# Optimization experiments

Measured on AMD Instinct MI355X. Metric: run time of the kernel, lower is better.

The kernel has to match this reference:

```python
import jax, jax.numpy as jnp
import numpy as np

BN_EPS = 1e-5
SMOOTH = 10.0


def l2norm(x, eps=1e-8):
    return x / (jnp.linalg.norm(x, axis=-1, keepdims=True) + eps)


def bn_tanh(z, gamma, beta):
    # BatchNorm1d in training mode (batch statistics, biased variance) + tanh
    mu = z.mean(axis=0)
    var = ((z - mu) ** 2).mean(axis=0)
    return jnp.tanh(gamma * (z - mu) / jnp.sqrt(var + BN_EPS) + beta)


def setup_inputs() -> dict:
    key = jax.random.key(0)
    ks = jax.random.split(key, 6)
    B, S, E, D = 1024, 512, 1024, 2048  # batch, att_num, embed_dim, image_dim
    return {
        "emb_instance": jax.random.normal(ks[0], (B, E), jnp.float32),
        "concept_feature": jax.random.normal(ks[1], (S, D), jnp.float32),
        "GT_label": jax.random.normal(ks[2], (B, S), jnp.float32),
        "fc1_w": jax.random.normal(ks[3], (D, E), jnp.float32) * 0.02,
        "fc1_b": jnp.zeros((E,), jnp.float32),
        "bn1_g": jnp.ones((E,), jnp.float32),
        "bn1_b": jnp.zeros((E,), jnp.float32),
        "fc2_w": jax.random.normal(ks[4], (E, E), jnp.float32) * 0.02,
        "fc2_b": jnp.zeros((E,), jnp.float32),
        "bn2_g": jnp.ones((E,), jnp.float32),
        "bn2_b": jnp.zeros((E,), jnp.float32),
        "fc3_w": jax.random.normal(ks[5], (E,), jnp.float32) * 0.02,
        "fc3_b": jnp.zeros((1,), jnp.float32),
        "GT_label_ratio": 0,
    }


def reference(emb_instance, concept_feature, GT_label, fc1_w, fc1_b, bn1_g, bn1_b,
              fc2_w, fc2_b, bn2_g, bn2_b, fc3_w, fc3_b, GT_label_ratio):
    # input_modal == 'visual' path
    W_s = bn_tanh(concept_feature @ fc1_w + fc1_b, bn1_g, bn1_b)   # (S, E)
    W_v = bn_tanh(emb_instance @ fc2_w + fc2_b, bn2_g, bn2_b)      # (B, E)
    # Fused bilinear score: fc3(W_s * W_v) == (W_v * fc3_w) @ W_s^T + fc3_b
    # avoids materializing the (B, S, E) broadcast intermediate.
    a_s = jnp.einsum('be,se->bs', W_v * fc3_w, W_s) + fc3_b        # (B, S)
    weights_v = jax.nn.softmax(a_s * SMOOTH, axis=1)
    cf = l2norm(concept_feature)                                    # (S, D)
    emb_concept = l2norm(weights_v @ cf)                            # (B, D)
    return (emb_concept, weights_v)
```

## Files before the change

kernel.cpp:

```cpp
#include <hip/hip_runtime.h>
#include <hip/hip_bf16.h>
#include <math.h>

#define B_ 1024
#define S_ 512
#define E_ 1024
#define D_ 2048
#define SMOOTH 10.0f

typedef __attribute__((ext_vector_type(8))) short bf16x8;
typedef __attribute__((ext_vector_type(4))) float f32x4;

__device__ __forceinline__ short f2bf(float f) {
    __hip_bfloat16 h = __float2bfloat16(f);
    short s; __builtin_memcpy(&s, &h, 2); return s;
}

__device__ __forceinline__ void gload16(const short* g, short* l) {
    __builtin_amdgcn_global_load_lds(
        (const __attribute__((address_space(1))) void*)(g),
        (__attribute__((address_space(3))) void*)(l), 16, 0, 0);
}

__inline__ __device__ float waveReduceMax(float v) {
#pragma unroll
    for (int o = 32; o; o >>= 1) v = fmaxf(v, __shfl_xor(v, o));
    return v;
}
__inline__ __device__ float waveReduceSum(float v) {
#pragma unroll
    for (int o = 32; o; o >>= 1) v += __shfl_xor(v, o);
    return v;
}

struct KArgs {
    const float *cf, *emb, *fc1w, *fc2w, *bn1g, *bn1b, *bn2g, *bn2b, *fc3w;
    short *A1, *A2, *Bt1, *Bt2, *cfT, *Ws, *Wv3, *A4;
    float *invn, *Z1, *Z2, *part1, *part2, *P1, *P2, *P3, *emb_pre;
    float *weights_v, *emb_concept;
};

__device__ __forceinline__ void transpose_bf(const float* __restrict__ in,
                                             short* __restrict__ out,
                                             int C, int r0, int c0, int ldo,
                                             int tid, float (*t)[33]) {
    int cx = tid & 31, ry0 = tid >> 5;
#pragma unroll
    for (int i = 0; i < 4; i++) {
        int ry = ry0 + i * 8;
        t[ry][cx] = in[(size_t)(r0 + ry) * C + c0 + cx];
    }
    __syncthreads();
    int rx = tid & 31, cy0 = tid >> 5;
#pragma unroll
    for (int i = 0; i < 4; i++) {
        int cy = cy0 + i * 8;
        out[(size_t)(c0 + cy) * ldo + r0 + rx] = f2bf(t[rx][cy]);
    }
}

__global__ __launch_bounds__(256) void prep_k(KArgs a) {
    __shared__ float t[32][33];
    __shared__ float red[4];
    const int task = blockIdx.x;
    const int tid = threadIdx.x;
    if (task < 512) {
        int row = task;
        const float* x = a.cf + (size_t)row * D_;
        short* aa = a.A1 + (size_t)row * D_;
        float ss = 0.f;
#pragma unroll
        for (int j = 0; j < 8; j++) {
            int i = j * 256 + tid;
            float v = x[i];
            aa[i] = f2bf(v);
            ss += v * v;
        }
        ss = waveReduceSum(ss);
        if ((tid & 63) == 0) red[tid >> 6] = ss;
        __syncthreads();
        if (tid == 0) {
            float s = red[0] + red[1] + red[2] + red[3];
            a.invn[row] = 1.0f / (sqrtf(s) + 1e-8f);
        }
    } else if (task < 1024) {
        int r0 = (task - 512) * 2;
#pragma unroll
        for (int rr = 0; rr < 2; rr++) {
            int row = r0 + rr;
            const float* x = a.emb + (size_t)row * E_;
            short* aa = a.A2 + (size_t)row * E_;
#pragma unroll
            for (int j = 0; j < 4; j++) {
                int i = j * 256 + tid;
                aa[i] = f2bf(x[i]);
            }
        }
    } else if (task < 3072) {
        int b2 = task - 1024;
        int c0 = (b2 & 31) * 32;
        int r0 = (b2 >> 5) * 32;
        transpose_bf(a.fc1w, a.Bt1, E_, r0, c0, D_, tid, t);
    } else if (task < 4096) {
        int b2 = task - 3072;
        int c0 = (b2 & 31) * 32;
        int r0 = (b2 >> 5) * 32;
        transpose_bf(a.fc2w, a.Bt2, E_, r0, c0, E_, tid, t);
    } else {
        int b2 = task - 4096;
        int c0 = (b2 & 63) * 32;
        int r0 = (b2 >> 6) * 32;
        transpose_bf(a.cf, a.cfT, D_, r0, c0, S_, tid, t);
    }
}

struct GP {
    const short* A;
    const short* Bm;
    float* P;
    int M, N, K, Kc, nx, ny;
};

__device__ __forceinline__ void gemm128_core(const GP g, int bid, short* lds) {
    const int tid = threadIdx.x;
    const int per = g.nx * g.ny;
    const int z = bid / per, rem = bid % per;
    const int by = rem / g.nx, bx = rem % g.nx;
    const int bm = by * 128, bn = bx * 128;
    const int kz = z * g.Kc;
    float* C = g.P + (size_t)z * g.M * g.N;
    const short* gA = g.A + (size_t)bm * g.K + kz;
    const short* gB = g.Bm + (size_t)bn * g.K + kz;

    size_t soff[4];
#pragma unroll
    for (int i = 0; i < 4; i++) {
        int ci = tid + i * 256;
        int row = ci >> 3, c = ci & 7;
        soff[i] = (size_t)row * g.K + ((c ^ (row & 7)) << 3);
    }

    auto stage = [&](int buf, int kt) {
        short* base = lds + buf * 16384;
#pragma unroll
        for (int i = 0; i < 4; i++) {
            gload16(gA + soff[i] + kt, base + tid * 8 + i * 2048);
            gload16(gB + soff[i] + kt, base + 8192 + tid * 8 + i * 2048);
        }
    };

    const int lane = tid & 63, wid = tid >> 6;
    const int wr = wid >> 1, wc = wid & 1;
    const int r16 = lane & 15, kg = lane >> 4;
    const int rs7 = (r16 & 7);

    f32x4 acc[4][4] = {};
    const int nt = g.Kc >> 6;

    stage(0, 0);
    for (int t = 0; t < nt; ++t) {
        __syncthreads();
        if (t + 1 < nt) stage((t + 1) & 1, (t + 1) << 6);
        const short* LA = lds + (t & 1) * 16384;
        const short* LB = LA + 8192;
#pragma unroll
        for (int ks = 0; ks < 2; ++ks) {
            const int sw = ((ks * 4 + kg) ^ rs7) << 3;
            bf16x8 a[4], b[4];
#pragma unroll
            for (int m = 0; m < 4; m++)
                a[m] = *(const bf16x8*)(LA + (wr * 64 + m * 16 + r16) * 64 + sw);
#pragma unroll
            for (int n = 0; n < 4; n++)
                b[n] = *(const bf16x8*)(LB + (wc * 64 + n * 16 + r16) * 64 + sw);
#pragma unroll
            for (int m = 0; m < 4; m++)
#pragma unroll
                for (int n = 0; n < 4; n++)
                    acc[m][n] = __builtin_amdgcn_mfma_f32_16x16x32_bf16(a[m], b[n], acc[m][n], 0, 0, 0);
        }
    }

#pragma unroll
    for (int m = 0; m < 4; m++)
#pragma unroll
        for (int n = 0; n < 4; n++) {
            int col = bn + wc * 64 + n * 16 + r16;
#pragma unroll
            for (int r = 0; r < 4; r++) {
                int row = bm + wr * 64 + m * 16 + kg * 4 + r;
                C[(size_t)row * g.N + col] = acc[m][n][r];
            }
        }
}

__global__ __launch_bounds__(256) void gemm_dual(GP g0, GP g1, int n0) {
    __shared__ short lds[32768];
    int bid = blockIdx.x;
    if (bid < n0) gemm128_core(g0, bid, lds);
    else gemm128_core(g1, bid - n0, lds);
}

__global__ __launch_bounds__(256) void gemm_one(GP g) {
    __shared__ short lds[32768];
    gemm128_core(g, blockIdx.x, lds);
}

__global__ __launch_bounds__(256) void bn_stats12(KArgs a) {
    int c = blockIdx.x * 256 + threadIdx.x;
    if (blockIdx.y < 32) {
        int r0 = blockIdx.y * 16;
        float s = 0.f, ss = 0.f;
        for (int r = r0; r < r0 + 16; r++) {
            float z = 0.f;
#pragma unroll
            for (int k = 0; k < 4; k++) z += a.P1[(size_t)k * S_ * E_ + (size_t)r * E_ + c];
            a.Z1[(size_t)r * E_ + c] = z;
            s += z; ss += z * z;
        }
        a.part1[(size_t)blockIdx.y * 2 * E_ + c] = s;
        a.part1[(size_t)blockIdx.y * 2 * E_ + E_ + c] = ss;
    } else {
        int y2 = blockIdx.y - 32;
        int r0 = y2 * 32;
        float s = 0.f, ss = 0.f;
        for (int r = r0; r < r0 + 32; r++) {
            float z = 0.f;
#pragma unroll
            for (int k = 0; k < 2; k++) z += a.P2[(size_t)k * B_ * E_ + (size_t)r * E_ + c];
            a.Z2[(size_t)r * E_ + c] = z;
            s += z; ss += z * z;
        }
        a.part2[(size_t)y2 * 2 * E_ + c] = s;
        a.part2[(size_t)y2 * 2 * E_ + E_ + c] = ss;
    }
}

__global__ __launch_bounds__(256) void bn_apply12(KArgs a) {
    int c = blockIdx.x * 256 + threadIdx.x;
    bool br1 = blockIdx.y < 32;
    const float* part = br1 ? a.part1 : a.part2;
    float s = 0.f, ss = 0.f;
#pragma unroll
    for (int k = 0; k < 32; k++) {
        s += part[(size_t)k * 2 * E_ + c];
        ss += part[(size_t)k * 2 * E_ + E_ + c];
    }
    float invR = br1 ? (1.0f / 512.0f) : (1.0f / 1024.0f);
    float mu = s * invR;
    float var = ss * invR - mu * mu;
    float rstd = rsqrtf(var + 1e-5f);
    float Aa = (br1 ? a.bn1g[c] : a.bn2g[c]) * rstd;
    float Bb = (br1 ? a.bn1b[c] : a.bn2b[c]) - Aa * mu;
    float sc = br1 ? 1.0f : a.fc3w[c];
    const float* Z = br1 ? a.Z1 : a.Z2;
    short* W = br1 ? a.Ws : a.Wv3;
    int nr = br1 ? 16 : 32;
    int r0 = (br1 ? blockIdx.y : (blockIdx.y - 32)) * nr;
    for (int r = r0; r < r0 + nr; r++) {
        float w = tanhf(fmaf(Z[(size_t)r * E_ + c], Aa, Bb)) * sc;
        W[(size_t)r * E_ + c] = f2bf(w);
    }
}

__global__ __launch_bounds__(256) void softmax_k(KArgs a) {
    __shared__ float red[4];
    int row = blockIdx.x;
    int tid = threadIdx.x;
    float v0 = 0.f, v1 = 0.f;
#pragma unroll
    for (int k = 0; k < 4; k++) {
        v0 += a.P3[(size_t)k * B_ * S_ + (size_t)row * S_ + tid];
        v1 += a.P3[(size_t)k * B_ * S_ + (size_t)row * S_ + tid + 256];
    }
    v0 *= SMOOTH;
    v1 *= SMOOTH;
    float m = waveReduceMax(fmaxf(v0, v1));
    if ((tid & 63) == 0) red[tid >> 6] = m;
    __syncthreads();
    m = fmaxf(fmaxf(red[0], red[1]), fmaxf(red[2], red[3]));
    float e0 = __expf(v0 - m), e1 = __expf(v1 - m);
    float s = waveReduceSum(e0 + e1);
    __syncthreads();
    if ((tid & 63) == 0) red[tid >> 6] = s;
    __syncthreads();
    s = red[0] + red[1] + red[2] + red[3];
    float inv = 1.0f / s;
    float w0 = e0 * inv, w1 = e1 * inv;
    a.weights_v[(size_t)row * S_ + tid] = w0;
    a.weights_v[(size_t)row * S_ + tid + 256] = w1;
    a.A4[(size_t)row * S_ + tid] = f2bf(w0 * a.invn[tid]);
    a.A4[(size_t)row * S_ + tid + 256] = f2bf(w1 * a.invn[tid + 256]);
}

__global__ __launch_bounds__(256) void rownorm_k(KArgs a) {
    __shared__ float red[4];
    int row = blockIdx.x;
    int tid = threadIdx.x;
    float v[8];
    float ss = 0.f;
#pragma unroll
    for (int j = 0; j < 8; j++) {
        v[j] = a.emb_pre[(size_t)row * D_ + j * 256 + tid];
        ss += v[j] * v[j];
    }
    ss = waveReduceSum(ss);
    if ((tid & 63) == 0) red[tid >> 6] = ss;
    __syncthreads();
    ss = red[0] + red[1] + red[2] + red[3];
    float sc = 1.0f / (sqrtf(ss) + 1e-8f);
#pragma unroll
    for (int j = 0; j < 8; j++)
        a.emb_concept[(size_t)row * D_ + j * 256 + tid] = v[j] * sc;
}

extern "C" void kernel_launch(void* const* d_in, const int* in_sizes, int n_in,
                              void* d_out, int out_size, void* d_ws, size_t ws_size,
                              hipStream_t stream) {
    float* out = (float*)d_out;
    const size_t MB = 1024 * 1024;
    char* w = (char*)d_ws;

    KArgs a;
    a.cf   = (const float*)d_in[1];
    a.emb  = (const float*)d_in[0];
    a.fc1w = (const float*)d_in[3];
    a.fc2w = (const float*)d_in[7];
    a.bn1g = (const float*)d_in[5];
    a.bn1b = (const float*)d_in[6];
    a.bn2g = (const float*)d_in[9];
    a.bn2b = (const float*)d_in[10];
    a.fc3w = (const float*)d_in[11];
    a.Bt1  = (short*)(w + 0 * MB);
    a.Bt2  = (short*)(w + 4 * MB);
    a.A1   = (short*)(w + 6 * MB);
    a.A2   = (short*)(w + 8 * MB);
    a.cfT  = (short*)(w + 10 * MB);
    a.Z1   = (float*)(w + 12 * MB);
    a.Z2   = (float*)(w + 14 * MB);
    a.Ws   = (short*)(w + 18 * MB);
    a.Wv3  = (short*)(w + 19 * MB);
    a.A4   = (short*)(w + 21 * MB);
    a.part1 = (float*)(w + 22 * MB);
    a.part2 = (float*)(w + 22 * MB + 512 * 1024);
    a.invn  = (float*)(w + 23 * MB);
    a.P1   = (float*)(w + 24 * MB);
    a.P2   = (float*)(w + 32 * MB);
    a.P3   = (float*)(w + 24 * MB);
    a.emb_pre = (float*)(w + 32 * MB);
    a.emb_concept = out;
    a.weights_v   = out + (size_t)B_ * D_;

    prep_k<<<5120, 256, 0, stream>>>(a);

    GP g1 = {a.A1, a.Bt1, a.P1, S_, E_, D_, 512, 8, 4};
    GP g2 = {a.A2, a.Bt2, a.P2, B_, E_, E_, 512, 8, 8};
    gemm_dual<<<256, 256, 0, stream>>>(g1, g2, 128);

    bn_stats12<<<dim3(4, 64), 256, 0, stream>>>(a);
    bn_apply12<<<dim3(4, 64), 256, 0, stream>>>(a);

    GP g3 = {a.Wv3, a.Ws, a.P3, B_, S_, E_, 256, 4, 8};
    gemm_one<<<128, 256, 0, stream>>>(g3);

    softmax_k<<<B_, 256, 0, stream>>>(a);

    GP g4 = {a.A4, a.cfT, a.emb_pre, B_, D_, S_, 512, 16, 8};
    gemm_one<<<128, 256, 0, stream>>>(g4);

    rownorm_k<<<B_, 256, 0, stream>>>(a);
}
```

Measured before the change: 74.80 us.

## Drop split-K in GEMMs, fuse BN stats/apply, halve prep grid

Removes the split-K partitioning from the fc1, fc2 and score GEMMs, so each block writes final outputs directly. This eliminates the partial-sum buffers and the reduction passes in BN stats and softmax. The two BN kernels are merged into one kernel that reduces column statistics in shared memory and then applies tanh. The prep kernel now runs each block over two tasks. The trade-off is far fewer GEMM blocks (96 and 32 on a GPU with many CUs), each with a longer K loop, which risks underutilising the device.

Result: slower. 103.9 us (+38.9%).

```diff
diff --git a/kernel.cpp b/kernel.cpp
--- a/kernel.cpp
+++ b/kernel.cpp
@@ -36,7 +36,7 @@
 struct KArgs {
     const float *cf, *emb, *fc1w, *fc2w, *bn1g, *bn1b, *bn2g, *bn2b, *fc3w;
     short *A1, *A2, *Bt1, *Bt2, *cfT, *Ws, *Wv3, *A4;
-    float *invn, *Z1, *Z2, *part1, *part2, *P1, *P2, *P3, *emb_pre;
+    float *invn, *Z1, *Z2, *a_s, *emb_pre;
     float *weights_v, *emb_concept;
 };
 
@@ -59,11 +59,8 @@
     }
 }
 
-__global__ __launch_bounds__(256) void prep_k(KArgs a) {
-    __shared__ float t[32][33];
-    __shared__ float red[4];
-    const int task = blockIdx.x;
-    const int tid = threadIdx.x;
+__device__ __forceinline__ void prep_task(const KArgs& a, int task, int tid,
+                                          float (*t)[33], float* red) {
     if (task < 512) {
         int row = task;
         const float* x = a.cf + (size_t)row * D_;
@@ -114,6 +111,15 @@
     }
 }
 
+__global__ __launch_bounds__(256) void prep_k(KArgs a) {
+    __shared__ float t[32][33];
+    __shared__ float red[4];
+    for (int it = 0; it < 2; ++it) {
+        prep_task(a, blockIdx.x + it * 2560, threadIdx.x, t, red);
+        __syncthreads();
+    }
+}
+
 struct GP {
     const short* A;
     const short* Bm;
@@ -206,58 +212,41 @@
     gemm128_core(g, blockIdx.x, lds);
 }
 
-__global__ __launch_bounds__(256) void bn_stats12(KArgs a) {
-    int c = blockIdx.x * 256 + threadIdx.x;
-    if (blockIdx.y < 32) {
-        int r0 = blockIdx.y * 16;
-        float s = 0.f, ss = 0.f;
-        for (int r = r0; r < r0 + 16; r++) {
-            float z = 0.f;
-#pragma unroll
-            for (int k = 0; k < 4; k++) z += a.P1[(size_t)k * S_ * E_ + (size_t)r * E_ + c];
-            a.Z1[(size_t)r * E_ + c] = z;
-            s += z; ss += z * z;
-        }
-        a.part1[(size_t)blockIdx.y * 2 * E_ + c] = s;
-        a.part1[(size_t)blockIdx.y * 2 * E_ + E_ + c] = ss;
-    } else {
-        int y2 = blockIdx.y - 32;
-        int r0 = y2 * 32;
-        float s = 0.f, ss = 0.f;
-        for (int r = r0; r < r0 + 32; r++) {
-            float z = 0.f;
-#pragma unroll
-            for (int k = 0; k < 2; k++) z += a.P2[(size_t)k * B_ * E_ + (size_t)r * E_ + c];
-            a.Z2[(size_t)r * E_ + c] = z;
-            s += z; ss += z * z;
-        }
-        a.part2[(size_t)y2 * 2 * E_ + c] = s;
-        a.part2[(size_t)y2 * 2 * E_ + E_ + c] = ss;
-    }
-}
-
-__global__ __launch_bounds__(256) void bn_apply12(KArgs a) {
-    int c = blockIdx.x * 256 + threadIdx.x;
-    bool br1 = blockIdx.y < 32;
-    const float* part = br1 ? a.part1 : a.part2;
+__global__ __launch_bounds__(256) void bn_fused(KArgs a) {
+    __shared__ float rs[16][16], rss[16][16];
+    __shared__ float sAa[16], sBb[16], sSc[16];
+    const int tid = threadIdx.x;
+    const int col = tid & 15, rg = tid >> 4;
+    const int c = blockIdx.x * 16 + col;
+    const bool br1 = (blockIdx.y == 0);
+    const float* Z = br1 ? a.Z1 : a.Z2;
+    const int R = br1 ? S_ : B_;
+
     float s = 0.f, ss = 0.f;
-#pragma unroll
-    for (int k = 0; k < 32; k++) {
-        s += part[(size_t)k * 2 * E_ + c];
-        ss += part[(size_t)k * 2 * E_ + E_ + c];
-    }
-    float invR = br1 ? (1.0f / 512.0f) : (1.0f / 1024.0f);
-    float mu = s * invR;
-    float var = ss * invR - mu * mu;
-    float rstd = rsqrtf(var + 1e-5f);
-    float Aa = (br1 ? a.bn1g[c] : a.bn2g[c]) * rstd;
-    float Bb = (br1 ? a.bn1b[c] : a.bn2b[c]) - Aa * mu;
-    float sc = br1 ? 1.0f : a.fc3w[c];
-    const float* Z = br1 ? a.Z1 : a.Z2;
+    for (int r = rg; r < R; r += 16) {
+        float z = Z[(size_t)r * E_ + c];
+        s += z; ss += z * z;
+    }
+    rs[rg][col] = s;
+    rss[rg][col] = ss;
+    __syncthreads();
+    if (rg == 0) {
+        float S = 0.f, SS = 0.f;
+#pragma unroll
+        for (int k = 0; k < 16; k++) { S += rs[k][col]; SS += rss[k][col]; }
+        float invR = 1.0f / (float)R;
+        float mu = S * invR;
+        float var = SS * invR - mu * mu;
+        float rstd = rsqrtf(var + 1e-5f);
+        float Aa = (br1 ? a.bn1g[c] : a.bn2g[c]) * rstd;
+        sAa[col] = Aa;
+        sBb[col] = (br1 ? a.bn1b[c] : a.bn2b[c]) - Aa * mu;
+        sSc[col] = br1 ? 1.0f : a.fc3w[c];
+    }
+    __syncthreads();
+    float Aa = sAa[col], Bb = sBb[col], sc = sSc[col];
     short* W = br1 ? a.Ws : a.Wv3;
-    int nr = br1 ? 16 : 32;
-    int r0 = (br1 ? blockIdx.y : (blockIdx.y - 32)) * nr;
-    for (int r = r0; r < r0 + nr; r++) {
+    for (int r = rg; r < R; r += 16) {
         float w = tanhf(fmaf(Z[(size_t)r * E_ + c], Aa, Bb)) * sc;
         W[(size_t)r * E_ + c] = f2bf(w);
     }
@@ -267,14 +256,8 @@
     __shared__ float red[4];
     int row = blockIdx.x;
     int tid = threadIdx.x;
-    float v0 = 0.f, v1 = 0.f;
-#pragma unroll
-    for (int k = 0; k < 4; k++) {
-        v0 += a.P3[(size_t)k * B_ * S_ + (size_t)row * S_ + tid];
-        v1 += a.P3[(size_t)k * B_ * S_ + (size_t)row * S_ + tid + 256];
-    }
-    v0 *= SMOOTH;
-    v1 *= SMOOTH;
+    float v0 = a.a_s[(size_t)row * S_ + tid] * SMOOTH;
+    float v1 = a.a_s[(size_t)row * S_ + tid + 256] * SMOOTH;
     float m = waveReduceMax(fmaxf(v0, v1));
     if ((tid & 63) == 0) red[tid >> 6] = m;
     __syncthreads();
@@ -341,31 +324,26 @@
     a.Ws   = (short*)(w + 18 * MB);
     a.Wv3  = (short*)(w + 19 * MB);
     a.A4   = (short*)(w + 21 * MB);
-    a.part1 = (float*)(w + 22 * MB);
-    a.part2 = (float*)(w + 22 * MB + 512 * 1024);
-    a.invn  = (float*)(w + 23 * MB);
-    a.P1   = (float*)(w + 24 * MB);
-    a.P2   = (float*)(w + 32 * MB);
-    a.P3   = (float*)(w + 24 * MB);
-    a.emb_pre = (float*)(w + 32 * MB);
+    a.invn = (float*)(w + 22 * MB);
+    a.a_s  = (float*)(w + 23 * MB);
+    a.emb_pre = (float*)(w + 25 * MB);
     a.emb_concept = out;
     a.weights_v   = out + (size_t)B_ * D_;
 
-    prep_k<<<5120, 256, 0, stream>>>(a);
-
-    GP g1 = {a.A1, a.Bt1, a.P1, S_, E_, D_, 512, 8, 4};
-    GP g2 = {a.A2, a.Bt2, a.P2, B_, E_, E_, 512, 8, 8};
-    gemm_dual<<<256, 256, 0, stream>>>(g1, g2, 128);
-
-    bn_stats12<<<dim3(4, 64), 256, 0, stream>>>(a);
-    bn_apply12<<<dim3(4, 64), 256, 0, stream>>>(a);
-
-    GP g3 = {a.Wv3, a.Ws, a.P3, B_, S_, E_, 256, 4, 8};
-    gemm_one<<<128, 256, 0, stream>>>(g3);
+    prep_k<<<2560, 256, 0, stream>>>(a);
+
+    GP g1 = {a.A1, a.Bt1, a.Z1, S_, E_, D_, D_, 8, 4};
+    GP g2 = {a.A2, a.Bt2, a.Z2, B_, E_, E_, E_, 8, 8};
+    gemm_dual<<<96, 256, 0, stream>>>(g1, g2, 32);
+
+    bn_fused<<<dim3(64, 2), 256, 0, stream>>>(a);
+
+    GP g3 = {a.Wv3, a.Ws, a.a_s, B_, S_, E_, E_, 4, 8};
+    gemm_one<<<32, 256, 0, stream>>>(g3);
 
     softmax_k<<<B_, 256, 0, stream>>>(a);
 
-    GP g4 = {a.A4, a.cfT, a.emb_pre, B_, D_, S_, 512, 16, 8};
+    GP g4 = {a.A4, a.cfT, a.emb_pre, B_, D_, S_, S_, 16, 8};
     gemm_one<<<128, 256, 0, stream>>>(g4);
 
     rownorm_k<<<B_, 256, 0, stream>>>(a);
```

## Replace split-K fc GEMMs with 64x128 tiles and fuse BN stats into epilogue

Applied to the files above, without the earlier changes.

The fc1/fc2 GEMMs switch from split-K 128x128 tiles to full-K 64x128 tiles. The epilogue writes Z directly and computes per-column partial sums and sums of squares through shuffles and LDS. This removes the split-K partial buffers and the separate bn_stats kernel that reduced them, saving a launch and a large amount of global traffic. The prep kernel and the transposes also move to vectorized 16-byte loads and 8-byte stores. In exchange, fc1 blocks now loop over the full K=2048 with only 192 blocks launched, which lowers parallelism and leaves fc1 and fc2 blocks with uneven amounts of work.

After: 73.77 us. Within noise of the previous version (-1.4%).

```diff
diff --git a/kernel.cpp b/kernel.cpp
--- a/kernel.cpp
+++ b/kernel.cpp
@@ -9,6 +9,7 @@
 #define SMOOTH 10.0f
 
 typedef __attribute__((ext_vector_type(8))) short bf16x8;
+typedef __attribute__((ext_vector_type(4))) short s16x4;
 typedef __attribute__((ext_vector_type(4))) float f32x4;
 
 __device__ __forceinline__ short f2bf(float f) {
@@ -36,7 +37,7 @@
 struct KArgs {
     const float *cf, *emb, *fc1w, *fc2w, *bn1g, *bn1b, *bn2g, *bn2b, *fc3w;
     short *A1, *A2, *Bt1, *Bt2, *cfT, *Ws, *Wv3, *A4;
-    float *invn, *Z1, *Z2, *part1, *part2, *P1, *P2, *P3, *emb_pre;
+    float *invn, *Z1, *Z2, *part1, *part2, *P3, *emb_pre;
     float *weights_v, *emb_concept;
 };
 
@@ -44,18 +45,19 @@
                                              short* __restrict__ out,
                                              int C, int r0, int c0, int ldo,
                                              int tid, float (*t)[33]) {
-    int cx = tid & 31, ry0 = tid >> 5;
-#pragma unroll
-    for (int i = 0; i < 4; i++) {
-        int ry = ry0 + i * 8;
-        t[ry][cx] = in[(size_t)(r0 + ry) * C + c0 + cx];
-    }
-    __syncthreads();
-    int rx = tid & 31, cy0 = tid >> 5;
-#pragma unroll
-    for (int i = 0; i < 4; i++) {
-        int cy = cy0 + i * 8;
-        out[(size_t)(c0 + cy) * ldo + r0 + rx] = f2bf(t[rx][cy]);
+    {
+        int r = tid >> 3, cq = tid & 7;
+        f32x4 v = *(const f32x4*)(in + (size_t)(r0 + r) * C + c0 + cq * 4);
+#pragma unroll
+        for (int i = 0; i < 4; i++) t[r][cq * 4 + i] = v[i];
+    }
+    __syncthreads();
+    {
+        int rq = tid & 7, cy = tid >> 3;
+        s16x4 o;
+#pragma unroll
+        for (int i = 0; i < 4; i++) o[i] = f2bf(t[rq * 4 + i][cy]);
+        *(s16x4*)(out + (size_t)(c0 + cy) * ldo + r0 + rq * 4) = o;
     }
 }
 
@@ -70,11 +72,13 @@
         short* aa = a.A1 + (size_t)row * D_;
         float ss = 0.f;
 #pragma unroll
-        for (int j = 0; j < 8; j++) {
-            int i = j * 256 + tid;
-            float v = x[i];
-            aa[i] = f2bf(v);
-            ss += v * v;
+        for (int j = 0; j < 2; j++) {
+            int i = (j * 256 + tid) * 4;
+            f32x4 v = *(const f32x4*)(x + i);
+            s16x4 o;
+#pragma unroll
+            for (int q = 0; q < 4; q++) { o[q] = f2bf(v[q]); ss += v[q] * v[q]; }
+            *(s16x4*)(aa + i) = o;
         }
         ss = waveReduceSum(ss);
         if ((tid & 63) == 0) red[tid >> 6] = ss;
@@ -88,13 +92,12 @@
 #pragma unroll
         for (int rr = 0; rr < 2; rr++) {
             int row = r0 + rr;
-            const float* x = a.emb + (size_t)row * E_;
-            short* aa = a.A2 + (size_t)row * E_;
-#pragma unroll
-            for (int j = 0; j < 4; j++) {
-                int i = j * 256 + tid;
-                aa[i] = f2bf(x[i]);
-            }
+            int i = tid * 4;
+            f32x4 v = *(const f32x4*)(a.emb + (size_t)row * E_ + i);
+            s16x4 o;
+#pragma unroll
+            for (int q = 0; q < 4; q++) o[q] = f2bf(v[q]);
+            *(s16x4*)(a.A2 + (size_t)row * E_ + i) = o;
         }
     } else if (task < 3072) {
         int b2 = task - 1024;
@@ -114,6 +117,135 @@
     }
 }
 
+struct GP64 {
+    const short* A;
+    const short* Bm;
+    float* Z;
+    float* part;
+    int M, N, K, nx;
+};
+
+__device__ __forceinline__ void gemm64_core(const GP64 g, int bid, short* lds) {
+    const int tid = threadIdx.x;
+    const int by = bid / g.nx, bx = bid % g.nx;
+    const int bm = by * 64, bn = bx * 128;
+    const short* gA = g.A + (size_t)bm * g.K;
+    const short* gB = g.Bm + (size_t)bn * g.K;
+
+    size_t aoff[2], boff[4];
+#pragma unroll
+    for (int i = 0; i < 2; i++) {
+        int ci = tid + i * 256;
+        int row = ci >> 3, c = ci & 7;
+        aoff[i] = (size_t)row * g.K + ((c ^ (row & 7)) << 3);
+    }
+#pragma unroll
+    for (int i = 0; i < 4; i++) {
+        int ci = tid + i * 256;
+        int row = ci >> 3, c = ci & 7;
+        boff[i] = (size_t)row * g.K + ((c ^ (row & 7)) << 3);
+    }
+
+    auto stage = [&](int buf, int kt) {
+        short* base = lds + buf * 12288;
+#pragma unroll
+        for (int i = 0; i < 2; i++)
+            gload16(gA + aoff[i] + kt, base + tid * 8 + i * 2048);
+#pragma unroll
+        for (int i = 0; i < 4; i++)
+            gload16(gB + boff[i] + kt, base + 4096 + tid * 8 + i * 2048);
+    };
+
+    const int lane = tid & 63, wid = tid >> 6;
+    const int wr = wid >> 1, wc = wid & 1;
+    const int r16 = lane & 15, kg = lane >> 4;
+    const int rs7 = r16 & 7;
+
+    f32x4 acc[2][4] = {};
+    const int nt = g.K >> 6;
+
+    stage(0, 0);
+    for (int t = 0; t < nt; ++t) {
+        __syncthreads();
+        if (t + 1 < nt) stage((t + 1) & 1, (t + 1) << 6);
+        const short* LA = lds + (t & 1) * 12288;
+        const short* LB = LA + 4096;
+#pragma unroll
+        for (int ks = 0; ks < 2; ++ks) {
+            const int sw = ((ks * 4 + kg) ^ rs7) << 3;
+            bf16x8 av[2], bv[4];
+#pragma unroll
+            for (int m = 0; m < 2; m++)
+                av[m] = *(const bf16x8*)(LA + (wr * 32 + m * 16 + r16) * 64 + sw);
+#pragma unroll
+            for (int n = 0; n < 4; n++)
+                bv[n] = *(const bf16x8*)(LB + (wc * 64 + n * 16 + r16) * 64 + sw);
+#pragma unroll
+            for (int m = 0; m < 2; m++)
+#pragma unroll
+                for (int n = 0; n < 4; n++)
+                    acc[m][n] = __builtin_amdgcn_mfma_f32_16x16x32_bf16(av[m], bv[n], acc[m][n], 0, 0, 0);
+        }
+    }
+
+#pragma unroll
+    for (int m = 0; m < 2; m++)
+#pragma unroll
+        for (int n = 0; n < 4; n++) {
+            int col = bn + wc * 64 + n * 16 + r16;
+#pragma unroll
+            for (int r = 0; r < 4; r++) {
+                int row = bm + wr * 32 + m * 16 + kg * 4 + r;
+                g.Z[(size_t)row * g.N + col] = acc[m][n][r];
+            }
+        }
+
+    float cs[4], cq[4];
+#pragma unroll
+    for (int n = 0; n < 4; n++) {
+        float s = 0.f, q = 0.f;
+#pragma unroll
+        for (int m = 0; m < 2; m++)
+#pragma unroll
+            for (int r = 0; r < 4; r++) {
+                float v = acc[m][n][r];
+                s += v; q += v * v;
+            }
+        cs[n] = s; cq[n] = q;
+    }
+#pragma unroll
+    for (int n = 0; n < 4; n++) {
+        cs[n] += __shfl_xor(cs[n], 16); cq[n] += __shfl_xor(cq[n], 16);
+        cs[n] += __shfl_xor(cs[n], 32); cq[n] += __shfl_xor(cq[n], 32);
+    }
+    __syncthreads();
+    float* sred = (float*)lds;
+    if (kg == 0) {
+#pragma unroll
+        for (int n = 0; n < 4; n++) {
+            int idx = (((wr * 2 + wc) * 4 + n) * 16 + r16) * 2;
+            sred[idx] = cs[n];
+            sred[idx + 1] = cq[n];
+        }
+    }
+    __syncthreads();
+    if (tid < 128) {
+        int wcc = tid >> 6, n = (tid >> 4) & 3, r = tid & 15;
+        int i0 = (((0 * 2 + wcc) * 4 + n) * 16 + r) * 2;
+        int i1 = (((1 * 2 + wcc) * 4 + n) * 16 + r) * 2;
+        int col = bn + wcc * 64 + n * 16 + r;
+        g.part[(size_t)by * 2 * g.N + col] = sred[i0] + sred[i1];
+        g.part[(size_t)by * 2 * g.N + g.N + col] = sred[i0 + 1] + sred[i1 + 1];
+    }
+}
+
+__global__ __launch_bounds__(256) void gemm_dual64(GP64 g0, GP64 g1, int n0) {
+    __shared__ short lds[24576];
+    int bid = blockIdx.x;
+    if (bid < n0) gemm64_core(g0, bid, lds);
+    else gemm64_core(g1, bid - n0, lds);
+}
+
 struct GP {
     const short* A;
     const short* Bm;
@@ -194,55 +326,18 @@
         }
 }
 
-__global__ __launch_bounds__(256) void gemm_dual(GP g0, GP g1, int n0) {
-    __shared__ short lds[32768];
-    int bid = blockIdx.x;
-    if (bid < n0) gemm128_core(g0, bid, lds);
-    else gemm128_core(g1, bid - n0, lds);
-}
-
 __global__ __launch_bounds__(256) void gemm_one(GP g) {
     __shared__ short lds[32768];
     gemm128_core(g, blockIdx.x, lds);
-}
-
-__global__ __launch_bounds__(256) void bn_stats12(KArgs a) {
-    int c = blockIdx.x * 256 + threadIdx.x;
-    if (blockIdx.y < 32) {
-        int r0 = blockIdx.y * 16;
-        float s = 0.f, ss = 0.f;
-        for (int r = r0; r < r0 + 16; r++) {
-            float z = 0.f;
-#pragma unroll
-            for (int k = 0; k < 4; k++) z += a.P1[(size_t)k * S_ * E_ + (size_t)r * E_ + c];
-            a.Z1[(size_t)r * E_ + c] = z;
-            s += z; ss += z * z;
-        }
-        a.part1[(size_t)blockIdx.y * 2 * E_ + c] = s;
-        a.part1[(size_t)blockIdx.y * 2 * E_ + E_ + c] = ss;
-    } else {
-        int y2 = blockIdx.y - 32;
-        int r0 = y2 * 32;
-        float s = 0.f, ss = 0.f;
-        for (int r = r0; r < r0 + 32; r++) {
-            float z = 0.f;
-#pragma unroll
-            for (int k = 0; k < 2; k++) z += a.P2[(size_t)k * B_ * E_ + (size_t)r * E_ + c];
-            a.Z2[(size_t)r * E_ + c] = z;
-            s += z; ss += z * z;
-        }
-        a.part2[(size_t)y2 * 2 * E_ + c] = s;
-        a.part2[(size_t)y2 * 2 * E_ + E_ + c] = ss;
-    }
 }
 
 __global__ __launch_bounds__(256) void bn_apply12(KArgs a) {
     int c = blockIdx.x * 256 + threadIdx.x;
     bool br1 = blockIdx.y < 32;
     const float* part = br1 ? a.part1 : a.part2;
+    int NS = br1 ? 8 : 16;
     float s = 0.f, ss = 0.f;
-#pragma unroll
-    for (int k = 0; k < 32; k++) {
+    for (int k = 0; k < NS; k++) {
         s += part[(size_t)k * 2 * E_ + c];
         ss += part[(size_t)k * 2 * E_ + E_ + c];
     }
@@ -336,16 +431,14 @@
     a.A1   = (short*)(w + 6 * MB);
     a.A2   = (short*)(w + 8 * MB);
     a.cfT  = (short*)(w + 10 * MB);
-    a.Z1   = (float*)(w + 12 * MB);
-    a.Z2   = (float*)(w + 14 * MB);
-    a.Ws   = (short*)(w + 18 * MB);
-    a.Wv3  = (short*)(w + 19 * MB);
-    a.A4   = (short*)(w + 21 * MB);
-    a.part1 = (float*)(w + 22 * MB);
-    a.part2 = (float*)(w + 22 * MB + 512 * 1024);
-    a.invn  = (float*)(w + 23 * MB);
-    a.P1   = (float*)(w + 24 * MB);
-    a.P2   = (float*)(w + 32 * MB);
+    a.Ws   = (short*)(w + 12 * MB);
+    a.Wv3  = (short*)(w + 13 * MB);
+    a.A4   = (short*)(w + 15 * MB);
+    a.invn = (float*)(w + 16 * MB);
+    a.Z1   = (float*)(w + 17 * MB);
+    a.Z2   = (float*)(w + 19 * MB);
+    a.part1 = (float*)(w + 23 * MB);
+    a.part2 = (float*)(w + 23 * MB + 256 * 1024);
     a.P3   = (float*)(w + 24 * MB);
     a.emb_pre = (float*)(w + 32 * MB);
     a.emb_concept = out;
@@ -353,11 +446,10 @@
 
     prep_k<<<5120, 256, 0, stream>>>(a);
 
-    GP g1 = {a.A1, a.Bt1, a.P1, S_, E_, D_, 512, 8, 4};
-    GP g2 = {a.A2, a.Bt2, a.P2, B_, E_, E_, 512, 8, 8};
-    gemm_dual<<<256, 256, 0, stream>>>(g1, g2, 128);
-
-    bn_stats12<<<dim3(4, 64), 256, 0, stream>>>(a);
+    GP64 g1 = {a.A1, a.Bt1, a.Z1, a.part1, S_, E_, D_, 8};
+    GP64 g2 = {a.A2, a.Bt2, a.Z2, a.part2, B_, E_, E_, 8};
+    gemm_dual64<<<192, 256, 0, stream>>>(g1, g2, 64);
+
     bn_apply12<<<dim3(4, 64), 256, 0, stream>>>(a);
 
     GP g3 = {a.Wv3, a.Ws, a.P3, B_, S_, E_, 256, 4, 8};
```
